# Optimization experiments

Measured on AMD Instinct MI355X. Metric: run time of the kernel, lower is better.

## Reference

```python
import jax, jax.numpy as jnp
import numpy as np

N_DST0 = 20000  # number of dst nodes of block0 == src nodes of block1


def _graph_conv(x, src, dst, n_dst, W, b):
    # DGL GraphConv with norm='both': D_in^{-1/2} A D_out^{-1/2} X W + b
    e_ones = jnp.ones(src.shape[0], dtype=x.dtype)
    deg_out = jax.ops.segment_sum(e_ones, src, num_segments=x.shape[0])
    deg_in = jax.ops.segment_sum(e_ones, dst, num_segments=n_dst)
    xs = x * jax.lax.rsqrt(jnp.maximum(deg_out, 1.0))[:, None]
    agg = jax.ops.segment_sum(xs[src], dst, num_segments=n_dst)  # [n_dst, F]
    agg = agg * jax.lax.rsqrt(jnp.maximum(deg_in, 1.0))[:, None]
    return agg @ W + b


def setup_inputs() -> dict:
    key = jax.random.key(0)
    ks = jax.random.split(key, 10)
    vocab, emb, hid, out = 50000, 128, 256, 16
    n_src0, n_dst0, n_dst1 = 50000, N_DST0, 5000
    e0, e1 = 300000, 75000
    return {
        "user_word": jax.random.randint(ks[0], (n_src0, 10, 5), 0, vocab),
        "labels": jax.random.randint(ks[1], (n_dst1,), 0, out),
        "src0": jax.random.randint(ks[2], (e0,), 0, n_src0),
        "dst0": jax.random.randint(ks[3], (e0,), 0, n_dst0),
        "src1": jax.random.randint(ks[4], (e1,), 0, n_dst0),
        "dst1": jax.random.randint(ks[5], (e1,), 0, n_dst1),
        "word_table": jax.random.normal(ks[6], (vocab, emb), jnp.float32),
        "W1": jax.random.normal(ks[7], (emb, hid), jnp.float32) * 0.05,
        "b1": jnp.zeros((hid,), jnp.float32),
        "W2": jax.random.normal(ks[8], (hid, out), jnp.float32) * 0.05,
        "b2": jnp.zeros((out,), jnp.float32),
    }


def reference(user_word, labels, src0, dst0, src1, dst1, word_table, W1, b1, W2, b2):
    n_dst1 = labels.shape[0]
    # embedding gather + mean over words (dim=2) then items (dim=1)
    wf = word_table[user_word]                    # [n_src0, n_items, n_words, emb]
    x = jnp.mean(jnp.mean(wf, axis=2), axis=1)    # [n_src0, emb]
    x = jax.nn.relu(_graph_conv(x, src0, dst0, N_DST0, W1, b1))
    x = jax.nn.relu(_graph_conv(x, src1, dst1, n_dst1, W2, b2))
    x = x[:n_dst1]
    return (x, labels)
```

## Files before the change

### kernel.cpp

```cpp
#include <hip/hip_runtime.h>

#define E0     300000
#define E1     75000
#define NSRC0  50000
#define NDST0  20000
#define NDST1  5000
#define EMB    128
#define HID    256
#define NOUT   16

#define NPB        40
#define TILE_SHIFT 12
#define NEMB_BLK   (NSRC0 / NPB)
#define NBKT_BLK   ((E0 + 255) / 256)

#define X0S  32.0f
#define H1S  64.0f

typedef __attribute__((ext_vector_type(8))) short bf16x8;
typedef __attribute__((ext_vector_type(4))) float f32x4;
typedef __attribute__((ext_vector_type(2))) float f32x2;

__device__ __forceinline__ unsigned short f2bf(float f) {
    unsigned u = __float_as_uint(f);
    return (unsigned short)((u + 0x7FFFu + ((u >> 16) & 1u)) >> 16);
}
__device__ __forceinline__ unsigned pack2(float a, float b) {
    return (unsigned)f2bf(a) | ((unsigned)f2bf(b) << 16);
}
__device__ __forceinline__ unsigned pack4_fp8(float a0, float a1, float a2, float a3) {
    unsigned p = 0;
    p = __builtin_amdgcn_cvt_pk_fp8_f32(a0, a1, p, false);
    p = __builtin_amdgcn_cvt_pk_fp8_f32(a2, a3, p, true);
    return p;
}
__device__ __forceinline__ unsigned char f2fp8(float v) {
    unsigned p = __builtin_amdgcn_cvt_pk_fp8_f32(v, v, 0, false);
    return (unsigned char)(p & 0xFF);
}
#if __has_builtin(__builtin_amdgcn_cvt_pk_f32_fp8)
__device__ __forceinline__ f32x2 up_lo(unsigned v) { return __builtin_amdgcn_cvt_pk_f32_fp8(v, false); }
__device__ __forceinline__ f32x2 up_hi(unsigned v) { return __builtin_amdgcn_cvt_pk_f32_fp8(v, true); }
#else
__device__ __forceinline__ f32x2 up_lo(unsigned v) {
    f32x2 r; r.x = __builtin_amdgcn_cvt_f32_fp8(v, 0); r.y = __builtin_amdgcn_cvt_f32_fp8(v, 1); return r;
}
__device__ __forceinline__ f32x2 up_hi(unsigned v) {
    f32x2 r; r.x = __builtin_amdgcn_cvt_f32_fp8(v, 2); r.y = __builtin_amdgcn_cvt_f32_fp8(v, 3); return r;
}
#endif

__global__ void prep_kernel(const float* __restrict__ wt, unsigned char* __restrict__ wt8,
                            const float* __restrict__ W1, unsigned short* __restrict__ W1Tb,
                            const float* __restrict__ W2, unsigned short* __restrict__ W2Tb,
                            const int* __restrict__ src0, const int* __restrict__ dst0,
                            const int* __restrict__ src1, const int* __restrict__ dst1,
                            int* cnt0, int* cnt1, int* degO0, int* degO1) {
    int i = blockIdx.x * blockDim.x + threadIdx.x;
    if (i < NSRC0 * EMB / 8) {
        const float4* in = (const float4*)wt;
        float4 v0 = in[i * 2], v1 = in[i * 2 + 1];
        uint2 o;
        o.x = pack4_fp8(v0.x, v0.y, v0.z, v0.w);
        o.y = pack4_fp8(v1.x, v1.y, v1.z, v1.w);
        ((uint2*)wt8)[i] = o;
    }
    if (i < EMB * HID) {
        int n = i & 255, k = i >> 8;
        W1Tb[n * 128 + k] = f2bf(W1[i]);
    }
    if (i < HID * NOUT) {
        int n = i & 15, k = i >> 4;
        W2Tb[n * 256 + k] = f2bf(W2[i]);
    }
    if (i < E0) {
        atomicAdd(&cnt0[dst0[i]], 1);
        atomicAdd(&degO0[src0[i]], 1);
    }
    if (i < E1) {
        atomicAdd(&cnt1[dst1[i]], 1);
        atomicAdd(&degO1[src1[i]], 1);
    }
}

__device__ void scan_body(const int* __restrict__ cnt, int n,
                          int* __restrict__ off, int* __restrict__ cur) {
    __shared__ int sums[1024];
    int t = threadIdx.x;
    int chunk = (n + 1023) / 1024;
    int lo = t * chunk, hi = min(lo + chunk, n);
    int s = 0;
    for (int i = lo; i < hi; ++i) s += cnt[i];
    sums[t] = s;
    __syncthreads();
    for (int d = 1; d < 1024; d <<= 1) {
        int x = (t >= d) ? sums[t - d] : 0;
        __syncthreads();
        sums[t] += x;
        __syncthreads();
    }
    int run = (t == 0) ? 0 : sums[t - 1];
    for (int i = lo; i < hi; ++i) {
        off[i] = run; cur[i] = run;
        run += cnt[i];
    }
    if (t == 1023) off[n] = run;
}

__global__ void scan_kernel(const int* cnt0, int* off0, int* cur0,
                            const int* cnt1, int* off1, int* cur1) {
    if (blockIdx.x == 0) scan_body(cnt0, NDST0, off0, cur0);
    else                 scan_body(cnt1, NDST1, off1, cur1);
}

__global__ void embed_bucket_kernel(const int* __restrict__ user_word,
                                    const unsigned char* __restrict__ wt8,
                                    const int* __restrict__ degO0,
                                    unsigned char* __restrict__ x0f,
                                    const int* __restrict__ src0, const int* __restrict__ dst0,
                                    const int* __restrict__ src1, const int* __restrict__ dst1,
                                    int* cur0, int* cur1, int* esrc0, int* esrc1) {
    if (blockIdx.x >= NEMB_BLK) {
        int i = (blockIdx.x - NEMB_BLK) * 256 + threadIdx.x;
        if (i < E0) {
            int p = atomicAdd(&cur0[dst0[i]], 1);
            esrc0[p] = src0[i];
        }
        if (i < E1) {
            int p = atomicAdd(&cur1[dst1[i]], 1);
            esrc1[p] = src1[i];
        }
        return;
    }
    __shared__ int raw[NPB * 50];
    __shared__ int srt[NPB * 50];
    __shared__ int cnt[NPB * 17];
    int t = threadIdx.x;
    int base = blockIdx.x * NPB * 50;
    for (int j = t; j < NPB * 50; j += 256)
        raw[j] = user_word[base + j];
    for (int j = t; j < NPB * 17; j += 256)
        cnt[j] = 0;
    __syncthreads();
    if (t < NPB) {
        int* c = cnt + t * 17;
        const int* r = raw + t * 50;
        for (int j = 0; j < 50; ++j) c[r[j] >> TILE_SHIFT]++;
        int run = 0;
        for (int b = 0; b < 13; ++b) { int v = c[b]; c[b] = run; run += v; }
        int* o = srt + t * 50;
        for (int j = 0; j < 50; ++j) { int v = r[j]; o[c[v >> TILE_SHIFT]++] = v; }
    }
    __syncthreads();
    int g = t >> 5, l = t & 31;
    const unsigned* wt4 = (const unsigned*)wt8;
    for (int n = g; n < NPB; n += 8) {
        const int* id = srt + n * 50;
        f32x2 a01 = {0.f, 0.f}, a23 = {0.f, 0.f};
        #pragma unroll 2
        for (int j = 0; j < 50; j += 2) {
            unsigned v0 = wt4[id[j] * 32 + l];
            unsigned v1 = wt4[id[j + 1] * 32 + l];
            a01 += up_lo(v0) + up_lo(v1);
            a23 += up_hi(v0) + up_hi(v1);
        }
        int node = blockIdx.x * NPB + n;
        float s = rsqrtf(fmaxf((float)degO0[node], 1.0f)) * (0.02f * X0S);
        ((unsigned*)x0f)[node * 32 + l] = pack4_fp8(a01.x * s, a01.y * s, a23.x * s, a23.y * s);
    }
}

__global__ void agg1_kernel(const int* __restrict__ off0, const int* __restrict__ esrc0,
                            const unsigned char* __restrict__ x0f,
                            unsigned short* __restrict__ agg1b) {
    int d = blockIdx.x;
    int t = threadIdx.x;
    int half = t >> 5, l = t & 31;
    int lo = off0[d], hi = off0[d + 1];
    const unsigned* x4 = (const unsigned*)x0f;
    f32x2 a01 = {0.f, 0.f}, a23 = {0.f, 0.f};
    for (int j = lo + half; j < hi; j += 2) {
        unsigned v = x4[esrc0[j] * 32 + l];
        a01 += up_lo(v); a23 += up_hi(v);
    }
    a01.x += __shfl_down(a01.x, 32); a01.y += __shfl_down(a01.y, 32);
    a23.x += __shfl_down(a23.x, 32); a23.y += __shfl_down(a23.y, 32);
    if (half == 0) {
        float sc = rsqrtf(fmaxf((float)(hi - lo), 1.0f)) * (1.0f / X0S);
        uint2 o; o.x = pack2(a01.x * sc, a01.y * sc); o.y = pack2(a23.x * sc, a23.y * sc);
        ((uint2*)agg1b)[d * 32 + l] = o;
    }
}

__global__ void gemm1_kernel(const unsigned short* __restrict__ agg1b,
                             const int* __restrict__ degO1,
                             const unsigned short* __restrict__ W1Tb,
                             const float* __restrict__ b1,
                             unsigned char* __restrict__ h1f) {
    __shared__ float s_out[16];
    int t = threadIdx.x;
    int row0 = blockIdx.x * 16;
    if (t < 16) s_out[t] = rsqrtf(fmaxf((float)degO1[row0 + t], 1.0f)) * H1S;
    __syncthreads();
    int w = t >> 6, lane = t & 63;
    int m = lane & 15, quad = lane >> 4;
    const unsigned short* abase = agg1b + (row0 + m) * 128 + quad * 8;
    bf16x8 afr[4];
    #pragma unroll
    for (int ks = 0; ks < 4; ++ks)
        afr[ks] = *(const bf16x8*)(abase + ks * 32);
    #pragma unroll
    for (int ct = 0; ct < 4; ++ct) {
        int gcol0 = (w * 4 + ct) * 16;
        const unsigned short* bbase = W1Tb + (gcol0 + m) * 128 + quad * 8;
        f32x4 acc = {0.f, 0.f, 0.f, 0.f};
        #pragma unroll
        for (int ks = 0; ks < 4; ++ks) {
            bf16x8 bfr = *(const bf16x8*)(bbase + ks * 32);
            acc = __builtin_amdgcn_mfma_f32_16x16x32_bf16(afr[ks], bfr, acc, 0, 0, 0);
        }
        int gcol = gcol0 + m;
        float bb = b1[gcol];
        #pragma unroll
        for (int reg = 0; reg < 4; ++reg) {
            int row = quad * 4 + reg;
            h1f[(row0 + row) * 256 + gcol] = f2fp8(fmaxf(acc[reg] + bb, 0.f) * s_out[row]);
        }
    }
}

__global__ void agg2_kernel(const int* __restrict__ off1, const int* __restrict__ esrc1,
                            const unsigned char* __restrict__ h1f,
                            unsigned short* __restrict__ agg2b) {
    int d = blockIdx.x;
    int l = threadIdx.x;
    int lo = off1[d], hi = off1[d + 1];
    const unsigned* h4 = (const unsigned*)h1f;
    f32x2 a01 = {0.f, 0.f}, a23 = {0.f, 0.f};
    int j = lo;
    for (; j + 1 < hi; j += 2) {
        unsigned v0 = h4[esrc1[j] * 64 + l];
        unsigned v1 = h4[esrc1[j + 1] * 64 + l];
        a01 += up_lo(v0) + up_lo(v1);
        a23 += up_hi(v0) + up_hi(v1);
    }
    if (j < hi) {
        unsigned v = h4[esrc1[j] * 64 + l];
        a01 += up_lo(v); a23 += up_hi(v);
    }
    float sc = rsqrtf(fmaxf((float)(hi - lo), 1.0f)) * (1.0f / H1S);
    uint2 o; o.x = pack2(a01.x * sc, a01.y * sc); o.y = pack2(a23.x * sc, a23.y * sc);
    ((uint2*)agg2b)[d * 64 + l] = o;
}

__global__ void gemm2_kernel(const unsigned short* __restrict__ agg2b,
                             const unsigned short* __restrict__ W2Tb,
                             const float* __restrict__ b2,
                             const int* __restrict__ labels,
                             float* __restrict__ out) {
    int lane = threadIdx.x;
    int row0 = blockIdx.x * 16;
    int m = lane & 15, quad = lane >> 4;
    int arow = min(row0 + m, NDST1 - 1);
    const unsigned short* abase = agg2b + arow * 256 + quad * 8;
    const unsigned short* bbase = W2Tb + m * 256 + quad * 8;
    f32x4 acc = {0.f, 0.f, 0.f, 0.f};
    #pragma unroll
    for (int ks = 0; ks < 8; ++ks) {
        bf16x8 af = *(const bf16x8*)(abase + ks * 32);
        bf16x8 bf = *(const bf16x8*)(bbase + ks * 32);
        acc = __builtin_amdgcn_mfma_f32_16x16x32_bf16(af, bf, acc, 0, 0, 0);
    }
    float bb = b2[m];
    #pragma unroll
    for (int reg = 0; reg < 4; ++reg) {
        int row = row0 + quad * 4 + reg;
        if (row < NDST1)
            out[row * NOUT + m] = fmaxf(acc[reg] + bb, 0.f);
    }
    if (lane < 16 && row0 + lane < NDST1)
        out[NDST1 * NOUT + row0 + lane] = (float)labels[row0 + lane];
}

extern "C" void kernel_launch(void* const* d_in, const int* in_sizes, int n_in,
                              void* d_out, int out_size, void* d_ws, size_t ws_size,
                              hipStream_t stream) {
    const int*   user_word  = (const int*)d_in[0];
    const int*   labels     = (const int*)d_in[1];
    const int*   src0       = (const int*)d_in[2];
    const int*   dst0       = (const int*)d_in[3];
    const int*   src1       = (const int*)d_in[4];
    const int*   dst1       = (const int*)d_in[5];
    const float* word_table = (const float*)d_in[6];
    const float* W1         = (const float*)d_in[7];
    const float* b1         = (const float*)d_in[8];
    const float* W2         = (const float*)d_in[9];
    const float* b2         = (const float*)d_in[10];

    int* iws = (int*)d_ws;
    int* cnt0  = iws;
    int* cnt1  = iws + 20000;
    int* degO0 = iws + 25000;
    int* degO1 = iws + 75000;
    int* off0  = iws + 95000;
    int* off1  = iws + 115001;
    int* cur0  = iws + 120002;
    int* cur1  = iws + 140002;
    int* esrc0 = iws + 145002;
    int* esrc1 = iws + 445002;
    unsigned char*  wt8   = (unsigned char*)(iws + 520004);
    unsigned char*  x0f   = (unsigned char*)(iws + 2120004);
    unsigned char*  h1f   = (unsigned char*)(iws + 3720004);
    unsigned short* agg1b = (unsigned short*)(iws + 5000004);
    unsigned short* agg2b = (unsigned short*)(iws + 6280004);
    unsigned short* W1Tb  = (unsigned short*)(iws + 6920004);
    unsigned short* W2Tb  = (unsigned short*)(iws + 6936388);

    hipMemsetAsync(iws, 0, 95000 * sizeof(int), stream);

    prep_kernel<<<(NSRC0 * EMB / 8 + 255) / 256, 256, 0, stream>>>(
        word_table, wt8, W1, W1Tb, W2, W2Tb,
        src0, dst0, src1, dst1, cnt0, cnt1, degO0, degO1);
    scan_kernel<<<2, 1024, 0, stream>>>(cnt0, off0, cur0, cnt1, off1, cur1);
    embed_bucket_kernel<<<NEMB_BLK + NBKT_BLK, 256, 0, stream>>>(
        user_word, wt8, degO0, x0f,
        src0, dst0, src1, dst1, cur0, cur1, esrc0, esrc1);
    agg1_kernel<<<NDST0, 64, 0, stream>>>(off0, esrc0, x0f, agg1b);
    gemm1_kernel<<<NDST0 / 16, 256, 0, stream>>>(agg1b, degO1, W1Tb, b1, h1f);
    agg2_kernel<<<NDST1, 64, 0, stream>>>(off1, esrc1, h1f, agg2b);
    gemm2_kernel<<<(NDST1 + 15) / 16, 64, 0, stream>>>(agg2b, W2Tb, b2, labels, (float*)d_out);
}
```

Baseline: 280.2 us.

## Interleave embedding gathers across nodes by vocab tile for cache locality

The embedding-mean kernel now assigns 10 nodes to each 64-lane wavefront and processes them in passes of 5. It walks vocab tiles in order, using the per-node bucket offsets, so that gathers from all 5 nodes hit the same region of the word table at the same time. The two 32-lane halves split each node's words and are combined with a cross-half shuffle. This aims for better L2/cache locality on table rows, at the cost of more loop overhead, more registers and divergent inner-loop trip counts.

```diff
diff --git a/kernel.cpp b/kernel.cpp
--- a/kernel.cpp
+++ b/kernel.cpp
@@ -152,21 +152,39 @@
         for (int j = 0; j < 50; ++j) { int v = r[j]; o[c[v >> TILE_SHIFT]++] = v; }
     }
     __syncthreads();
-    int g = t >> 5, l = t & 31;
+    int w = t >> 6;
+    int lane = t & 63, half = lane >> 5, l = lane & 31;
     const unsigned* wt4 = (const unsigned*)wt8;
-    for (int n = g; n < NPB; n += 8) {
-        const int* id = srt + n * 50;
-        f32x2 a01 = {0.f, 0.f}, a23 = {0.f, 0.f};
-        #pragma unroll 2
-        for (int j = 0; j < 50; j += 2) {
-            unsigned v0 = wt4[id[j] * 32 + l];
-            unsigned v1 = wt4[id[j + 1] * 32 + l];
-            a01 += up_lo(v0) + up_lo(v1);
-            a23 += up_hi(v0) + up_hi(v1);
-        }
-        int node = blockIdx.x * NPB + n;
-        float s = rsqrtf(fmaxf((float)degO0[node], 1.0f)) * (0.02f * X0S);
-        ((unsigned*)x0f)[node * 32 + l] = pack4_fp8(a01.x * s, a01.y * s, a23.x * s, a23.y * s);
+    #pragma unroll
+    for (int pass = 0; pass < 2; ++pass) {
+        int n0 = w * 10 + pass * 5;
+        f32x2 a01[5], a23[5];
+        #pragma unroll
+        for (int k = 0; k < 5; ++k) { a01[k] = (f32x2){0.f, 0.f}; a23[k] = (f32x2){0.f, 0.f}; }
+        for (int b = 0; b < 13; ++b) {
+            #pragma unroll
+            for (int k = 0; k < 5; ++k) {
+                int n = n0 + k;
+                int js = b ? cnt[n * 17 + b - 1] : 0;
+                int je = cnt[n * 17 + b];
+                const int* id = srt + n * 50;
+                for (int j = js + half; j < je; j += 2) {
+                    unsigned v = wt4[id[j] * 32 + l];
+                    a01[k] += up_lo(v); a23[k] += up_hi(v);
+                }
+            }
+        }
+        #pragma unroll
+        for (int k = 0; k < 5; ++k) {
+            a01[k].x += __shfl_down(a01[k].x, 32); a01[k].y += __shfl_down(a01[k].y, 32);
+            a23[k].x += __shfl_down(a23[k].x, 32); a23[k].y += __shfl_down(a23[k].y, 32);
+            if (half == 0) {
+                int node = blockIdx.x * NPB + n0 + k;
+                float s = rsqrtf(fmaxf((float)degO0[node], 1.0f)) * (0.02f * X0S);
+                ((unsigned*)x0f)[node * 32 + l] =
+                    pack4_fp8(a01[k].x * s, a01[k].y * s, a23[k].x * s, a23[k].y * s);
+            }
+        }
     }
 }
 
```

Result: slower. 315.3 us (+12.5%).

## Interleave bucketing blocks with embedding blocks and gather five nodes per warp

Applied to the files above, without the earlier changes.

Edge-bucketing blocks now take the odd block indices and embedding blocks the even ones, rather than running as a trailing range. The intent is for the atomic-heavy bucketing work to run alongside the latency-bound embedding gathers instead of after them. The embedding gather loop also processes all five of a warp's nodes together, issuing five independent word-table loads per step to raise memory-level parallelism. The cost is more accumulator registers, which may lower occupancy, and a changed access order across the tile-sorted word ids.

```diff
diff --git a/kernel.cpp b/kernel.cpp
--- a/kernel.cpp
+++ b/kernel.cpp
@@ -12,7 +12,6 @@
 #define NPB        40
 #define TILE_SHIFT 12
 #define NEMB_BLK   (NSRC0 / NPB)
-#define NBKT_BLK   ((E0 + 255) / 256)
 
 #define X0S  32.0f
 #define H1S  64.0f
@@ -120,8 +119,8 @@
                                     const int* __restrict__ src0, const int* __restrict__ dst0,
                                     const int* __restrict__ src1, const int* __restrict__ dst1,
                                     int* cur0, int* cur1, int* esrc0, int* esrc1) {
-    if (blockIdx.x >= NEMB_BLK) {
-        int i = (blockIdx.x - NEMB_BLK) * 256 + threadIdx.x;
+    if (blockIdx.x & 1) {
+        int i = (blockIdx.x >> 1) * 256 + threadIdx.x;
         if (i < E0) {
             int p = atomicAdd(&cur0[dst0[i]], 1);
             esrc0[p] = src0[i];
@@ -132,11 +131,12 @@
         }
         return;
     }
+    int eb = blockIdx.x >> 1;
     __shared__ int raw[NPB * 50];
     __shared__ int srt[NPB * 50];
     __shared__ int cnt[NPB * 17];
     int t = threadIdx.x;
-    int base = blockIdx.x * NPB * 50;
+    int base = eb * NPB * 50;
     for (int j = t; j < NPB * 50; j += 256)
         raw[j] = user_word[base + j];
     for (int j = t; j < NPB * 17; j += 256)
@@ -154,19 +154,32 @@
     __syncthreads();
     int g = t >> 5, l = t & 31;
     const unsigned* wt4 = (const unsigned*)wt8;
-    for (int n = g; n < NPB; n += 8) {
-        const int* id = srt + n * 50;
-        f32x2 a01 = {0.f, 0.f}, a23 = {0.f, 0.f};
-        #pragma unroll 2
-        for (int j = 0; j < 50; j += 2) {
-            unsigned v0 = wt4[id[j] * 32 + l];
-            unsigned v1 = wt4[id[j + 1] * 32 + l];
-            a01 += up_lo(v0) + up_lo(v1);
-            a23 += up_hi(v0) + up_hi(v1);
-        }
-        int node = blockIdx.x * NPB + n;
+    const int* id0 = srt + (g     ) * 50;
+    const int* id1 = srt + (g +  8) * 50;
+    const int* id2 = srt + (g + 16) * 50;
+    const int* id3 = srt + (g + 24) * 50;
+    const int* id4 = srt + (g + 32) * 50;
+    f32x2 a01[5], a23[5];
+    #pragma unroll
+    for (int k = 0; k < 5; ++k) { a01[k] = (f32x2){0.f, 0.f}; a23[k] = (f32x2){0.f, 0.f}; }
+    for (int j = 0; j < 50; ++j) {
+        unsigned v0 = wt4[id0[j] * 32 + l];
+        unsigned v1 = wt4[id1[j] * 32 + l];
+        unsigned v2 = wt4[id2[j] * 32 + l];
+        unsigned v3 = wt4[id3[j] * 32 + l];
+        unsigned v4 = wt4[id4[j] * 32 + l];
+        a01[0] += up_lo(v0); a23[0] += up_hi(v0);
+        a01[1] += up_lo(v1); a23[1] += up_hi(v1);
+        a01[2] += up_lo(v2); a23[2] += up_hi(v2);
+        a01[3] += up_lo(v3); a23[3] += up_hi(v3);
+        a01[4] += up_lo(v4); a23[4] += up_hi(v4);
+    }
+    #pragma unroll
+    for (int k = 0; k < 5; ++k) {
+        int node = eb * NPB + g + k * 8;
         float s = rsqrtf(fmaxf((float)degO0[node], 1.0f)) * (0.02f * X0S);
-        ((unsigned*)x0f)[node * 32 + l] = pack4_fp8(a01.x * s, a01.y * s, a23.x * s, a23.y * s);
+        ((unsigned*)x0f)[node * 32 + l] =
+            pack4_fp8(a01[k].x * s, a01[k].y * s, a23[k].x * s, a23[k].y * s);
     }
 }
 
@@ -322,7 +335,7 @@
         word_table, wt8, W1, W1Tb, W2, W2Tb,
         src0, dst0, src1, dst1, cnt0, cnt1, degO0, degO1);
     scan_kernel<<<2, 1024, 0, stream>>>(cnt0, off0, cur0, cnt1, off1, cur1);
-    embed_bucket_kernel<<<NEMB_BLK + NBKT_BLK, 256, 0, stream>>>(
+    embed_bucket_kernel<<<NEMB_BLK * 2, 256, 0, stream>>>(
         user_word, wt8, degO0, x0f,
         src0, dst0, src1, dst1, cur0, cur1, esrc0, esrc1);
     agg1_kernel<<<NDST0, 64, 0, stream>>>(off0, esrc0, x0f, agg1b);
```

After: 268.4 us. -4.2%, faster.
